# Optimization experiments

Hardware: AMD Instinct MI355X
Metric: run time of the kernel (lower is better)

Reference implementation:

```python
import jax, jax.numpy as jnp
import numpy as np

B, MSTEP, NFEAT, ATT = 8192, 200, 64, 64

def setup_inputs() -> dict:
    key = jax.random.key(0)
    k1, k2, k3, k4, k5, k6 = jax.random.split(key, 6)
    sc_q = (6.0 / (NFEAT + ATT)) ** 0.5
    sc_s = (6.0 / (ATT + 1)) ** 0.5
    return {
        "x": jax.random.normal(k1, (B, NFEAT), dtype=jnp.float32),
        "mem": jax.random.normal(k2, (B, MSTEP, NFEAT), dtype=jnp.float32),
        "Wq": jax.random.uniform(k3, (NFEAT, ATT), jnp.float32, -sc_q, sc_q),
        "Wk": jax.random.uniform(k4, (NFEAT, ATT), jnp.float32, -sc_q, sc_q),
        "bias": jax.random.uniform(k5, (ATT,), jnp.float32, -sc_q, sc_q),
        "Ws": jax.random.uniform(k6, (ATT, 1), jnp.float32, -sc_s, sc_s),
    }

def reference(x, mem, Wq, Wk, bias, Ws):
    # query: [B, 1, att]
    query = (x @ Wq)[:, None, :]
    # key: [B, mstep, att]
    key = jnp.einsum("bmf,fa->bma", mem, Wk)
    # additive attention: tanh(q + k + b), scalar score, softmax over mstep
    proj = jnp.tanh(query + key + bias)
    scores = jnp.einsum("bma,ao->bm", proj, Ws)          # [B, mstep]
    weights = jax.nn.softmax(scores, axis=1)              # softmax over mstep
    # context: weighted sum of keys -> [B, att]
    context = jnp.einsum("bm,bma->ba", weights, key)
    return context
```

## Files before the change

kernel.cpp:

```cpp
#include <hip/hip_runtime.h>
#include <math.h>

#define MSTEP 200
#define NF 64
#define NA 64
#define MROWS 208
#define NMT 13

typedef __bf16 bf16x4 __attribute__((ext_vector_type(4)));
typedef __bf16 bf16x8 __attribute__((ext_vector_type(8)));
typedef float  floatx4 __attribute__((ext_vector_type(4)));


__launch_bounds__(256, 2)
__global__ void customAttention_48515950576474_kernel(
    const float* __restrict__ x, const float* __restrict__ mem,
    const float* __restrict__ Wq, const float* __restrict__ Wk,
    const float* __restrict__ bias, const float* __restrict__ Ws,
    float* __restrict__ out)
{
    __shared__ __align__(16) __bf16 mh[MROWS * NF];
    __shared__ __align__(16) __bf16 ml[MROWS * NF];
    __shared__ __align__(16) __bf16 wh[NA * NF];
    __shared__ __align__(16) __bf16 wl[NA * NF];
    __shared__ float q_lds[NA];
    __shared__ float scores[MROWS];
    __shared__ float weights[MROWS];
    __shared__ float ctxp[4][NA];
    __shared__ float redmax[4], redsum[4];

    const int t    = threadIdx.x;
    const int b    = blockIdx.x;
    const int w    = t >> 6;
    const int lane = t & 63;

    const float4* memb4 = (const float4*)(mem + (size_t)b * (MSTEP * NF));
    for (int it = 0; it < 13; ++it) {
        int fi = t + (it << 8);
        if (fi < MSTEP * 16) {
            float4 v = memb4[fi];
            int m = fi >> 4, qq = fi & 15;
            int eo = m * 64 + (((qq >> 1) ^ (m & 7)) << 3) + ((qq & 1) << 2);
            float vv[4] = {v.x, v.y, v.z, v.w};
            bf16x4 h, l;
            #pragma unroll
            for (int j = 0; j < 4; ++j) {
                __bf16 hb = (__bf16)vv[j];
                h[j] = hb;
                l[j] = (__bf16)(vv[j] - (float)hb);
            }
            *(bf16x4*)&mh[eo] = h;
            *(bf16x4*)&ml[eo] = l;
        }
    }
    if (t < 64) {
        int m = MSTEP + (t >> 3), c = t & 7;
        int eo = m * 64 + ((c ^ (m & 7)) << 3);
        *(float4*)&mh[eo] = make_float4(0.f, 0.f, 0.f, 0.f);
        *(float4*)&ml[eo] = make_float4(0.f, 0.f, 0.f, 0.f);
    }

    for (int i = 0; i < 16; ++i) {
        int idx = t + (i << 8);
        int kk = idx >> 6, a = idx & 63;
        float v = Wk[idx];
        __bf16 hb = (__bf16)v;
        int eo = a * 64 + ((((kk >> 3) ^ (a & 7))) << 3) + (kk & 7);
        wh[eo] = hb;
        wl[eo] = (__bf16)(v - (float)hb);
    }

    {
        float xv = x[(size_t)b * NF + lane];
        int aj = lane & 15, fh = lane >> 4;
        int a0 = w << 4;
        float qp = 0.f;
        #pragma unroll
        for (int kx = 0; kx < 16; ++kx) {
            int ff = fh * 16 + kx;
            qp = fmaf(__shfl(xv, ff), Wq[ff * NA + a0 + aj], qp);
        }
        qp += __shfl_xor(qp, 16);
        qp += __shfl_xor(qp, 32);
        if (fh == 0) q_lds[a0 + aj] = qp + bias[a0 + aj];
    }
    __syncthreads();

    bf16x8 bh[4][2], bl[4][2];
    {
        int a = lane & 15, ko = lane >> 4;
        #pragma unroll
        for (int at = 0; at < 4; ++at) {
            int row = at * 16 + a;
            #pragma unroll
            for (int kc = 0; kc < 2; ++kc) {
                int eo = row * 64 + (((kc * 4 + ko) ^ (row & 7)) << 3);
                bh[at][kc] = *(const bf16x8*)&wh[eo];
                bl[at][kc] = *(const bf16x8*)&wl[eo];
            }
        }
    }

    floatx4 kreg[4][4];
    #pragma unroll
    for (int i = 0; i < 4; ++i)
        #pragma unroll
        for (int at = 0; at < 4; ++at)
            kreg[i][at] = (floatx4){0.f, 0.f, 0.f, 0.f};

    float qv[4], wsv[4];
    #pragma unroll
    for (int at = 0; at < 4; ++at) {
        int a = at * 16 + (lane & 15);
        qv[at]  = q_lds[a];
        wsv[at] = Ws[a];
    }

    #pragma unroll
    for (int i = 0; i < 4; ++i) {
        int mt = w + 4 * i;
        if (mt < NMT) {
            int m = mt * 16 + (lane & 15);
            int ko = lane >> 4;
            bf16x8 ah[2], al[2];
            #pragma unroll
            for (int kc = 0; kc < 2; ++kc) {
                int eo = m * 64 + (((kc * 4 + ko) ^ (m & 7)) << 3);
                ah[kc] = *(const bf16x8*)&mh[eo];
                al[kc] = *(const bf16x8*)&ml[eo];
            }
            #pragma unroll
            for (int at = 0; at < 4; ++at) {
                floatx4 acc = kreg[i][at];
                #pragma unroll
                for (int kc = 0; kc < 2; ++kc) {
                    acc = __builtin_amdgcn_mfma_f32_16x16x32_bf16(ah[kc], bh[at][kc], acc, 0, 0, 0);
                    acc = __builtin_amdgcn_mfma_f32_16x16x32_bf16(ah[kc], bl[at][kc], acc, 0, 0, 0);
                    acc = __builtin_amdgcn_mfma_f32_16x16x32_bf16(al[kc], bh[at][kc], acc, 0, 0, 0);
                }
                kreg[i][at] = acc;
            }
            float s[4] = {0.f, 0.f, 0.f, 0.f};
            #pragma unroll
            for (int at = 0; at < 4; ++at) {
                #pragma unroll
                for (int r = 0; r < 4; ++r) {
                    float e  = __expf(2.f * (kreg[i][at][r] + qv[at]));
                    float th = 1.f - 2.f / (e + 1.f);
                    s[r] = fmaf(th, wsv[at], s[r]);
                }
            }
            #pragma unroll
            for (int r = 0; r < 4; ++r) {
                s[r] += __shfl_xor(s[r], 1);
                s[r] += __shfl_xor(s[r], 2);
                s[r] += __shfl_xor(s[r], 4);
                s[r] += __shfl_xor(s[r], 8);
            }
            if ((lane & 15) == 0) {
                int mrow = mt * 16 + (lane >> 4) * 4;
                scores[mrow + 0] = s[0];
                scores[mrow + 1] = s[1];
                scores[mrow + 2] = s[2];
                scores[mrow + 3] = s[3];
            }
        }
    }
    __syncthreads();

    {
        float sv = (t < MSTEP) ? scores[t] : -INFINITY;
        float mx = sv;
        #pragma unroll
        for (int d = 1; d < 64; d <<= 1) mx = fmaxf(mx, __shfl_xor(mx, d));
        if (lane == 0) redmax[w] = mx;
        __syncthreads();
        mx = fmaxf(fmaxf(redmax[0], redmax[1]), fmaxf(redmax[2], redmax[3]));
        float e = (t < MSTEP) ? __expf(sv - mx) : 0.f;
        float sm = e;
        #pragma unroll
        for (int d = 1; d < 64; d <<= 1) sm += __shfl_xor(sm, d);
        if (lane == 0) redsum[w] = sm;
        __syncthreads();
        float tot = redsum[0] + redsum[1] + redsum[2] + redsum[3];
        if (t < MROWS) weights[t] = e / tot;
    }
    __syncthreads();

    {
        float c[4] = {0.f, 0.f, 0.f, 0.f};
        #pragma unroll
        for (int i = 0; i < 4; ++i) {
            int mt = w + 4 * i;
            if (mt < NMT) {
                int mrow = mt * 16 + (lane >> 4) * 4;
                #pragma unroll
                for (int r = 0; r < 4; ++r) {
                    float wv = weights[mrow + r];
                    #pragma unroll
                    for (int at = 0; at < 4; ++at)
                        c[at] = fmaf(wv, kreg[i][at][r], c[at]);
                }
            }
        }
        #pragma unroll
        for (int at = 0; at < 4; ++at) {
            c[at] += __shfl_xor(c[at], 16);
            c[at] += __shfl_xor(c[at], 32);
        }
        if (lane < 16) {
            #pragma unroll
            for (int at = 0; at < 4; ++at)
                ctxp[w][at * 16 + lane] = c[at];
        }
    }
    __syncthreads();

    if (t < NA)
        out[(size_t)b * NA + t] = ctxp[0][t] + ctxp[1][t] + ctxp[2][t] + ctxp[3][t];
}

extern "C" void kernel_launch(void* const* d_in, const int* in_sizes, int n_in,
                              void* d_out, int out_size, void* d_ws, size_t ws_size,
                              hipStream_t stream) {
    const float* x    = (const float*)d_in[0];
    const float* mem  = (const float*)d_in[1];
    const float* Wq   = (const float*)d_in[2];
    const float* Wk   = (const float*)d_in[3];
    const float* bias = (const float*)d_in[4];
    const float* Ws   = (const float*)d_in[5];
    float* out = (float*)d_out;
    const int B = in_sizes[0] / NF;
    customAttention_48515950576474_kernel<<<B, 256, 0, stream>>>(x, mem, Wq, Wk, bias, Ws, out);
}
```

Measured before the change: 655.5 us.

## Load mem directly into MFMA registers, drop LDS staging, and fuse softmax

```diff
diff --git a/kernel.cpp b/kernel.cpp
--- a/kernel.cpp
+++ b/kernel.cpp
@@ -4,68 +4,38 @@
 #define MSTEP 200
 #define NF 64
 #define NA 64
-#define MROWS 208
 #define NMT 13
 
-typedef __bf16 bf16x4 __attribute__((ext_vector_type(4)));
 typedef __bf16 bf16x8 __attribute__((ext_vector_type(8)));
 typedef float  floatx4 __attribute__((ext_vector_type(4)));
 
 
-__launch_bounds__(256, 2)
+__launch_bounds__(256, 3)
 __global__ void customAttention_48515950576474_kernel(
     const float* __restrict__ x, const float* __restrict__ mem,
     const float* __restrict__ Wq, const float* __restrict__ Wk,
     const float* __restrict__ bias, const float* __restrict__ Ws,
     float* __restrict__ out)
 {
-    __shared__ __align__(16) __bf16 mh[MROWS * NF];
-    __shared__ __align__(16) __bf16 ml[MROWS * NF];
     __shared__ __align__(16) __bf16 wh[NA * NF];
     __shared__ __align__(16) __bf16 wl[NA * NF];
     __shared__ float q_lds[NA];
-    __shared__ float scores[MROWS];
-    __shared__ float weights[MROWS];
+    __shared__ float scores[NMT * 16];
     __shared__ float ctxp[4][NA];
-    __shared__ float redmax[4], redsum[4];
 
     const int t    = threadIdx.x;
     const int b    = blockIdx.x;
     const int w    = t >> 6;
     const int lane = t & 63;
 
-    const float4* memb4 = (const float4*)(mem + (size_t)b * (MSTEP * NF));
-    for (int it = 0; it < 13; ++it) {
-        int fi = t + (it << 8);
-        if (fi < MSTEP * 16) {
-            float4 v = memb4[fi];
-            int m = fi >> 4, qq = fi & 15;
-            int eo = m * 64 + (((qq >> 1) ^ (m & 7)) << 3) + ((qq & 1) << 2);
-            float vv[4] = {v.x, v.y, v.z, v.w};
-            bf16x4 h, l;
-            #pragma unroll
-            for (int j = 0; j < 4; ++j) {
-                __bf16 hb = (__bf16)vv[j];
-                h[j] = hb;
-                l[j] = (__bf16)(vv[j] - (float)hb);
-            }
-            *(bf16x4*)&mh[eo] = h;
-            *(bf16x4*)&ml[eo] = l;
-        }
-    }
-    if (t < 64) {
-        int m = MSTEP + (t >> 3), c = t & 7;
-        int eo = m * 64 + ((c ^ (m & 7)) << 3);
-        *(float4*)&mh[eo] = make_float4(0.f, 0.f, 0.f, 0.f);
-        *(float4*)&ml[eo] = make_float4(0.f, 0.f, 0.f, 0.f);
-    }
+    const float* memb = mem + (size_t)b * (MSTEP * NF);
 
     for (int i = 0; i < 16; ++i) {
         int idx = t + (i << 8);
         int kk = idx >> 6, a = idx & 63;
         float v = Wk[idx];
         __bf16 hb = (__bf16)v;
-        int eo = a * 64 + ((((kk >> 3) ^ (a & 7))) << 3) + (kk & 7);
+        int eo = a * 64 + (((kk >> 3) ^ (a & 7)) << 3) + (kk & 7);
         wh[eo] = hb;
         wl[eo] = (__bf16)(v - (float)hb);
     }
@@ -94,19 +64,12 @@
             int row = at * 16 + a;
             #pragma unroll
             for (int kc = 0; kc < 2; ++kc) {
-                int eo = row * 64 + (((kc * 4 + ko) ^ (row & 7)) << 3);
+                int eo = row * 64 + ((((kc * 4 + ko)) ^ (row & 7)) << 3);
                 bh[at][kc] = *(const bf16x8*)&wh[eo];
                 bl[at][kc] = *(const bf16x8*)&wl[eo];
             }
         }
     }
-
-    floatx4 kreg[4][4];
-    #pragma unroll
-    for (int i = 0; i < 4; ++i)
-        #pragma unroll
-        for (int at = 0; at < 4; ++at)
-            kreg[i][at] = (floatx4){0.f, 0.f, 0.f, 0.f};
 
     float qv[4], wsv[4];
     #pragma unroll
@@ -116,18 +79,36 @@
         wsv[at] = Ws[a];
     }
 
+    floatx4 kreg[4][4];
+    #pragma unroll
+    for (int i = 0; i < 4; ++i)
+        #pragma unroll
+        for (int at = 0; at < 4; ++at)
+            kreg[i][at] = (floatx4){0.f, 0.f, 0.f, 0.f};
+
     #pragma unroll
     for (int i = 0; i < 4; ++i) {
         int mt = w + 4 * i;
         if (mt < NMT) {
-            int m = mt * 16 + (lane & 15);
+            int m  = mt * 16 + (lane & 15);
             int ko = lane >> 4;
+            bool valid = (m < MSTEP);
             bf16x8 ah[2], al[2];
             #pragma unroll
             for (int kc = 0; kc < 2; ++kc) {
-                int eo = m * 64 + (((kc * 4 + ko) ^ (m & 7)) << 3);
-                ah[kc] = *(const bf16x8*)&mh[eo];
-                al[kc] = *(const bf16x8*)&ml[eo];
+                const float* ap = memb + m * 64 + kc * 32 + ko * 8;
+                float4 p0 = valid ? *(const float4*)ap       : make_float4(0.f, 0.f, 0.f, 0.f);
+                float4 p1 = valid ? *(const float4*)(ap + 4) : make_float4(0.f, 0.f, 0.f, 0.f);
+                float vv[8] = {p0.x, p0.y, p0.z, p0.w, p1.x, p1.y, p1.z, p1.w};
+                bf16x8 h, l;
+                #pragma unroll
+                for (int j = 0; j < 8; ++j) {
+                    __bf16 hb = (__bf16)vv[j];
+                    h[j] = hb;
+                    l[j] = (__bf16)(vv[j] - (float)hb);
+                }
+                ah[kc] = h;
+                al[kc] = l;
             }
             #pragma unroll
             for (int at = 0; at < 4; ++at) {
@@ -168,24 +149,21 @@
     }
     __syncthreads();
 
-    {
-        float sv = (t < MSTEP) ? scores[t] : -INFINITY;
-        float mx = sv;
+    float mx, inv;
+    {
+        float s0 = scores[lane];
+        float s1 = scores[lane + 64];
+        float s2 = scores[lane + 128];
+        float s3 = (lane < 8) ? scores[lane + 192] : -INFINITY;
+        mx = fmaxf(fmaxf(s0, s1), fmaxf(s2, s3));
         #pragma unroll
         for (int d = 1; d < 64; d <<= 1) mx = fmaxf(mx, __shfl_xor(mx, d));
-        if (lane == 0) redmax[w] = mx;
-        __syncthreads();
-        mx = fmaxf(fmaxf(redmax[0], redmax[1]), fmaxf(redmax[2], redmax[3]));
-        float e = (t < MSTEP) ? __expf(sv - mx) : 0.f;
-        float sm = e;
-        #pragma unroll
-        for (int d = 1; d < 64; d <<= 1) sm += __shfl_xor(sm, d);
-        if (lane == 0) redsum[w] = sm;
-        __syncthreads();
-        float tot = redsum[0] + redsum[1] + redsum[2] + redsum[3];
-        if (t < MROWS) weights[t] = e / tot;
-    }
-    __syncthreads();
+        float e = __expf(s0 - mx) + __expf(s1 - mx) + __expf(s2 - mx)
+                + ((lane < 8) ? __expf(s3 - mx) : 0.f);
+        #pragma unroll
+        for (int d = 1; d < 64; d <<= 1) e += __shfl_xor(e, d);
+        inv = 1.0f / e;
+    }
 
     {
         float c[4] = {0.f, 0.f, 0.f, 0.f};
@@ -196,7 +174,8 @@
                 int mrow = mt * 16 + (lane >> 4) * 4;
                 #pragma unroll
                 for (int r = 0; r < 4; ++r) {
-                    float wv = weights[mrow + r];
+                    float wv = (mrow + r < MSTEP)
+                             ? __expf(scores[mrow + r] - mx) * inv : 0.f;
                     #pragma unroll
                     for (int at = 0; at < 4; ++at)
                         c[at] = fmaf(wv, kreg[i][at][r], c[at]);
```

Measured after the change: 589.3 us. -10.1%, faster.
